# Optimization experiments

Hardware: AMD Instinct MI355X
Metric: run time of the kernel (lower is better)

Reference implementation:

```python
import jax, jax.numpy as jnp
import numpy as np

B, S, D = 4, 1024, 1024
H, DK, DH = 16, 64, 64  # num_heads, key_size, head_size
NEG = 1e12


def setup_inputs() -> dict:
    key = jax.random.key(0)
    ks = jax.random.split(key, 16)
    scale = 0.02
    inp = {
        'q': jax.random.normal(ks[0], (B, S, D), jnp.float32),
        'k': jax.random.normal(ks[1], (B, S, D), jnp.float32),
        'v': jax.random.normal(ks[2], (B, S, D), jnp.float32),
        'v_mask': jax.random.randint(ks[3], (B, S), 0, 2, jnp.int32),
        'q_mask': jax.random.randint(ks[4], (B, S), 0, 2, jnp.int32),
        # causal attention mask (float, 1 = keep)
        'a_mask': jnp.tril(jnp.ones((S, S), jnp.float32))[None, None, :, :],
        'Wq': jax.random.normal(ks[5], (D, H * DK), jnp.float32) * scale,
        'bq': jnp.zeros((H * DK,), jnp.float32),
        'Wk': jax.random.normal(ks[6], (D, H * DK), jnp.float32) * scale,
        'bk': jnp.zeros((H * DK,), jnp.float32),
        'Wv': jax.random.normal(ks[7], (D, H * DH), jnp.float32) * scale,
        'bv': jnp.zeros((H * DH,), jnp.float32),
        'Wo': jax.random.normal(ks[8], (H * DH, H * DH), jnp.float32) * scale,
        'bo': jnp.zeros((H * DH,), jnp.float32),
    }
    return inp


def reference(q, k, v, v_mask, q_mask, a_mask, Wq, bq, Wk, bk, Wv, bv, Wo, bo):
    b, sq, _ = q.shape
    sk = k.shape[1]
    qw = (jnp.einsum('bsd,de->bse', q, Wq) + bq).reshape(b, sq, H, DK)
    kw = (jnp.einsum('bsd,de->bse', k, Wk) + bk).reshape(b, sk, H, DK)
    vw = (jnp.einsum('bsd,de->bse', v, Wv) + bv).reshape(b, sk, H, DH)
    # scores [b, h, sq, sk]
    a = jnp.einsum('bjhd,bkhd->bhjk', qw, kw) / jnp.sqrt(jnp.float32(DK))
    vm = v_mask.astype(jnp.float32)  # [b, sk]
    a = a - (1.0 - vm)[:, None, None, :] * NEG  # sequence_masking mode='add'
    a = a - (1.0 - a_mask) * NEG                # attention mask
    p = jax.nn.softmax(a, axis=-1)
    o = jnp.einsum('bhjk,bkhd->bjhd', p, vw).reshape(b, sq, H * DH)
    o = jnp.einsum('bse,ef->bsf', o, Wo) + bo
    qm = q_mask.astype(jnp.float32)
    o = o * qm[:, :, None]  # sequence_masking mode='mul'
    return o
```

## Files before the change

### kernel.cpp

```cpp
#include <hip/hip_runtime.h>
#include <cstdint>
#include <cstddef>

typedef unsigned short u16;
using short8 = __attribute__((ext_vector_type(8))) short;
using f32x4  = __attribute__((ext_vector_type(4))) float;

constexpr int Sc = 1024;
constexpr float PEN = 60.0f;

__device__ __forceinline__ u16 f2bf(float f) {
  union { float f; uint32_t u; } v; v.f = f;
  return (u16)((v.u + 0x7fffu + ((v.u >> 16) & 1u)) >> 16);
}

__device__ __forceinline__ void gload_lds16(const u16* g, u16* l) {
  __builtin_amdgcn_global_load_lds(
      (const __attribute__((address_space(1))) uint32_t*)g,
      (__attribute__((address_space(3))) uint32_t*)l, 16, 0, 0);
}

__device__ __forceinline__ f32x4 mfma16(short8 a, short8 b, f32x4 c) {
  return __builtin_amdgcn_mfma_f32_16x16x32_bf16(a, b, c, 0, 0, 0);
}

__global__ __launch_bounds__(256) void prep(
    const float* __restrict__ q, const float* __restrict__ k,
    const float* __restrict__ v, u16* __restrict__ qb, u16* __restrict__ kb,
    u16* __restrict__ vb, const float* __restrict__ W0,
    const float* __restrict__ W1, const float* __restrict__ W2,
    const float* __restrict__ W3, u16* __restrict__ D0, u16* __restrict__ D1,
    u16* __restrict__ D2, u16* __restrict__ D3) {
  const int y = blockIdx.y;
  if (y < 3) {
    const float* src = y == 0 ? q : y == 1 ? k : v;
    u16* dst = y == 0 ? qb : y == 1 ? kb : vb;
    int i = blockIdx.x * 256 + threadIdx.x;
    float4 a = ((const float4*)src)[2 * i];
    float4 b = ((const float4*)src)[2 * i + 1];
    u16 t[8] = {f2bf(a.x), f2bf(a.y), f2bf(a.z), f2bf(a.w),
                f2bf(b.x), f2bf(b.y), f2bf(b.z), f2bf(b.w)};
    ((uint4*)dst)[i] = *(const uint4*)t;
  } else {
    if (blockIdx.x >= 1024) return;
    const int z = y - 3;
    const float* W = z == 0 ? W0 : z == 1 ? W1 : z == 2 ? W2 : W3;
    u16* WT = z == 0 ? D0 : z == 1 ? D1 : z == 2 ? D2 : D3;
    __shared__ float t[32][33];
    int bx = (blockIdx.x & 31) * 32, by = (blockIdx.x >> 5) * 32;
    int tx = threadIdx.x & 31, ty = threadIdx.x >> 5;
    for (int i = 0; i < 32; i += 8)
      t[ty + i][tx] = W[(size_t)(by + ty + i) * 1024 + bx + tx];
    __syncthreads();
    for (int i = 0; i < 32; i += 8)
      WT[(size_t)(bx + ty + i) * 1024 + by + tx] = f2bf(t[tx][ty + i]);
  }
}

__global__ __launch_bounds__(256, 6) void gemm_qkv(
    const u16* __restrict__ qb, const u16* __restrict__ kb,
    const u16* __restrict__ vb, const u16* __restrict__ BT,
    const float* __restrict__ bq, const float* __restrict__ bk,
    const float* __restrict__ bv, u16* __restrict__ QW, u16* __restrict__ KW,
    u16* __restrict__ VTg) {
  const int bid = blockIdx.x;
  const int xcd = bid & 7, local = bid >> 3;
  const int mp = local & 3, nbi = local >> 2;
  const int m0 = (xcd * 4 + mp) * 128, n0 = nbi * 64;
  const int seg = nbi >> 4;
  const u16* A    = seg == 0 ? qb : seg == 1 ? kb : vb;
  const float* bias = seg == 0 ? bq : seg == 1 ? bk : bv;

  __shared__ u16 As0[128 * 32], As1[128 * 32];
  __shared__ u16 Bs0[64 * 32], Bs1[64 * 32];

  const int t = threadIdx.x, w = t >> 6, lane = t & 63;
  const int q4 = lane >> 4, lm = lane & 15;
  const int wm = (w >> 1) * 64, wn = (w & 1) * 32;
  const int srow = lane >> 2, p = lane & 3;
  const int cf = q4 ^ ((lm >> 2) & 3);

  const int rbA0 = (w * 2) * 16, rbA1 = (w * 2 + 1) * 16, rbB = w * 16;
  const int rowA0 = rbA0 + srow, rowA1 = rbA1 + srow, rowB = rbB + srow;
  const int cA0 = p ^ ((rowA0 >> 2) & 3), cA1 = p ^ ((rowA1 >> 2) & 3);
  const int cB = p ^ ((rowB >> 2) & 3);
  const u16* pa0 = &A[(size_t)(m0 + rowA0) * 1024 + cA0 * 8];
  const u16* pa1 = &A[(size_t)(m0 + rowA1) * 1024 + cA1 * 8];
  const u16* pb  = &BT[(size_t)(n0 + rowB) * 1024 + cB * 8];

  f32x4 acc[4][2] = {};

  auto stage = [&](u16* as, u16* bs) {
    gload_lds16(pa0, as + rbA0 * 32);
    gload_lds16(pa1, as + rbA1 * 32);
    gload_lds16(pb, bs + rbB * 32);
    pa0 += 32; pa1 += 32; pb += 32;
  };
  auto compute = [&](const u16* as, const u16* bs) {
    short8 af[4], bf[2];
    for (int mi = 0; mi < 4; ++mi)
      af[mi] = *(const short8*)&as[(wm + mi * 16 + lm) * 32 + cf * 8];
    for (int ni = 0; ni < 2; ++ni)
      bf[ni] = *(const short8*)&bs[(wn + ni * 16 + lm) * 32 + cf * 8];
    for (int mi = 0; mi < 4; ++mi)
      for (int ni = 0; ni < 2; ++ni)
        acc[mi][ni] = mfma16(af[mi], bf[ni], acc[mi][ni]);
  };

  stage(As0, Bs0);
  for (int it = 0; it < 16; ++it) {
    __syncthreads();
    stage(As1, Bs1);
    compute(As0, Bs0);
    __syncthreads();
    if (it < 15) stage(As0, Bs0);
    compute(As1, Bs1);
  }

  if (seg < 2) {
    u16* C = seg == 0 ? QW : KW;
    for (int mi = 0; mi < 4; ++mi)
      for (int ni = 0; ni < 2; ++ni)
        for (int r = 0; r < 4; ++r) {
          int row = m0 + wm + mi * 16 + q4 * 4 + r;
          int col = (n0 + wn + ni * 16 + lm) & 1023;
          C[(size_t)row * 1024 + col] = f2bf(acc[mi][ni][r] + bias[col]);
        }
  } else {
    for (int mi = 0; mi < 4; ++mi)
      for (int ni = 0; ni < 2; ++ni) {
        int row0 = m0 + wm + mi * 16 + q4 * 4;
        int col = (n0 + wn + ni * 16 + lm) & 1023;
        float bv4 = bias[col];
        u16 o4[4];
        for (int r = 0; r < 4; ++r) o4[r] = f2bf(acc[mi][ni][r] + bv4);
        *(uint2*)&VTg[(size_t)col * 4096 + row0] = *(const uint2*)o4;
      }
  }
}

__global__ __launch_bounds__(256, 4) void gemm_out(
    const u16* __restrict__ A, const u16* __restrict__ BT,
    const float* __restrict__ bias, const int* __restrict__ qmask,
    float* __restrict__ Cf) {
  const int bid = blockIdx.x;
  const int xcd = bid & 7, local = bid >> 3;
  const int mp = local & 7, nb = local >> 3;
  const int m0 = (xcd * 8 + mp) * 64, n0 = nb * 64;

  __shared__ u16 As0[64 * 32], As1[64 * 32];
  __shared__ u16 Bs0[64 * 32], Bs1[64 * 32];
  const int t = threadIdx.x, w = t >> 6, lane = t & 63;
  const int q4 = lane >> 4, lm = lane & 15;
  const int wm = (w >> 1) * 32, wn = (w & 1) * 32;
  const int srow = lane >> 2, p = lane & 3;
  const int cf = q4 ^ ((lm >> 2) & 3);

  const int rb = w * 16;
  const int rowS = rb + srow;
  const int cS = p ^ ((rowS >> 2) & 3);
  const u16* pa = &A[(size_t)(m0 + rowS) * 1024 + cS * 8];
  const u16* pb = &BT[(size_t)(n0 + rowS) * 1024 + cS * 8];

  f32x4 acc[2][2] = {};

  auto stage = [&](u16* as, u16* bs) {
    gload_lds16(pa, as + rb * 32);
    gload_lds16(pb, bs + rb * 32);
    pa += 32; pb += 32;
  };
  auto compute = [&](const u16* as, const u16* bs) {
    short8 af[2], bf[2];
    for (int mi = 0; mi < 2; ++mi)
      af[mi] = *(const short8*)&as[(wm + mi * 16 + lm) * 32 + cf * 8];
    for (int ni = 0; ni < 2; ++ni)
      bf[ni] = *(const short8*)&bs[(wn + ni * 16 + lm) * 32 + cf * 8];
    for (int mi = 0; mi < 2; ++mi)
      for (int ni = 0; ni < 2; ++ni)
        acc[mi][ni] = mfma16(af[mi], bf[ni], acc[mi][ni]);
  };

  stage(As0, Bs0);
  for (int it = 0; it < 16; ++it) {
    __syncthreads();
    stage(As1, Bs1);
    compute(As0, Bs0);
    __syncthreads();
    if (it < 15) stage(As0, Bs0);
    compute(As1, Bs1);
  }

  for (int mi = 0; mi < 2; ++mi)
    for (int ni = 0; ni < 2; ++ni)
      for (int r = 0; r < 4; ++r) {
        int row = m0 + wm + mi * 16 + q4 * 4 + r;
        int col = n0 + wn + ni * 16 + lm;
        Cf[(size_t)row * 1024 + col] =
            (acc[mi][ni][r] + bias[col]) * (float)qmask[row];
      }
}

__global__ __launch_bounds__(256) void attn(
    const u16* __restrict__ QW, const u16* __restrict__ KW,
    const u16* __restrict__ VTg, const int* __restrict__ vmask,
    u16* __restrict__ O) {
  const int bid = blockIdx.x;
  const int xcd = bid & 7, local = bid >> 3;
  const int pair = xcd * 8 + (local & 7);
  const int b = pair >> 4, h = pair & 15;
  const int bx = local >> 3;
  const int qta = bx, qtb = 15 - bx;
  const int t = threadIdx.x, w = t >> 6, lane = t & 63;
  const int q4 = lane >> 4, lm = lane & 15;

  __shared__ u16 Ks[2][64 * 64];
  __shared__ u16 VTs[2][64 * 64];
  __shared__ u16 P[4][16 * 88];
  __shared__ float penv[1024];
  __shared__ int anyf[2];

  if (t < 2) anyf[t] = 0;
  {
    int4 vm = ((const int4*)(vmask + b * 1024))[t];
    penv[4 * t + 0] = (1.f - (float)vm.x) * PEN;
    penv[4 * t + 1] = (1.f - (float)vm.y) * PEN;
    penv[4 * t + 2] = (1.f - (float)vm.z) * PEN;
    penv[4 * t + 3] = (1.f - (float)vm.w) * PEN;
  }
  __syncthreads();
  {
    int any_a = 0, any_b = 0;
    for (int i = t; i <= qtb * 64; i += 256) {
      int un = (penv[i] == 0.f);
      if (i <= qta * 64) any_a |= un;
      any_b |= un;
    }
    if (any_a) atomicOr(&anyf[0], 1);
    if (any_b) atomicOr(&anyf[1], 1);
  }
  __syncthreads();
  const int extA = !anyf[0], extB = !anyf[1];
  const int kend = (extA || extB) ? 15 : qtb;

  short8 qf[2][2];
  for (int s = 0; s < 2; ++s) {
    int qt = s ? qtb : qta;
    const u16* qp = &QW[(size_t)(b * Sc + qt * 64 + w * 16 + lm) * 1024 + h * 64];
    qf[s][0] = *(const short8*)&qp[q4 * 8];
    qf[s][1] = *(const short8*)&qp[32 + q4 * 8];
    for (int fi = 0; fi < 2; ++fi)
      for (int i = 0; i < 8; ++i) {
        u16 x = (u16)qf[s][fi][i];
        int e = (x >> 7) & 0xff;
        qf[s][fi][i] = (short)(e > 3 ? (u16)(x - 0x180) : (u16)(x & 0x8000));
      }
  }

  float l_run[2][4] = {};
  f32x4 oacc[2][4] = {};

  const int r0 = lane >> 3, pos = lane & 7, ch = pos ^ r0;
  auto stage = [&](int kt, int buf) {
    for (int j = 0; j < 2; ++j) {
      int issue = w * 2 + j;
      int row = issue * 8 + r0;
      gload_lds16(&KW[(size_t)(b * Sc + kt * 64 + row) * 1024 + h * 64 + ch * 8],
                  &Ks[buf][issue * 512]);
      gload_lds16(&VTg[(size_t)(h * 64 + row) * 4096 + b * Sc + kt * 64 + ch * 8],
                  &VTs[buf][issue * 512]);
    }
  };

  auto strip_tile = [&](int s, int kt, int mode, int buf) {
    const int qt = s ? qtb : qta;
    const int qrow0 = qt * 64 + w * 16 + q4 * 4;
    f32x4 sacc[4] = {};
    for (int ni = 0; ni < 4; ++ni) {
      int row = ni * 16 + lm;
      short8 kf0 = *(const short8*)&Ks[buf][row * 64 + ((q4 ^ (lm & 7)) * 8)];
      short8 kf1 = *(const short8*)&Ks[buf][row * 64 + (((4 + q4) ^ (lm & 7)) * 8)];
      sacc[ni] = mfma16(qf[s][0], kf0, sacc[ni]);
      sacc[ni] = mfma16(qf[s][1], kf1, sacc[ni]);
    }
    u16* Pw = &P[w][0];
    for (int ni = 0; ni < 4; ++ni) {
      int key = kt * 64 + ni * 16 + lm;
      float pen = penv[key];
      if (mode == 2) pen += PEN;
      for (int r = 0; r < 4; ++r) {
        float x = sacc[ni][r] - pen;
        if (mode == 1 && key > qrow0 + r) x -= PEN;
        float pv = __expf(x);
        l_run[s][r] += pv;
        Pw[(q4 * 4 + r) * 88 + ni * 16 + lm] = f2bf(pv);
      }
    }
    short8 pf0 = *(const short8*)&Pw[lm * 88 + q4 * 8];
    short8 pf1 = *(const short8*)&Pw[lm * 88 + 32 + q4 * 8];
    for (int ni = 0; ni < 4; ++ni) {
      int row = ni * 16 + lm;
      short8 vf0 = *(const short8*)&VTs[buf][row * 64 + ((q4 ^ (lm & 7)) * 8)];
      short8 vf1 = *(const short8*)&VTs[buf][row * 64 + (((4 + q4) ^ (lm & 7)) * 8)];
      oacc[s][ni] = mfma16(pf0, vf0, oacc[s][ni]);
      oacc[s][ni] = mfma16(pf1, vf1, oacc[s][ni]);
    }
  };

  stage(0, 0);
  int cur = 0;
  for (int kt = 0; kt <= kend; ++kt) {
    __syncthreads();
    if (kt < kend) stage(kt + 1, cur ^ 1);
    if (kt <= qta) strip_tile(0, kt, kt == qta ? 1 : 0, cur);
    else if (extA) strip_tile(0, kt, 2, cur);
    if (kt <= qtb) strip_tile(1, kt, kt == qtb ? 1 : 0, cur);
    else if (extB) strip_tile(1, kt, 2, cur);
    cur ^= 1;
  }

  for (int s = 0; s < 2; ++s) {
    int qt = s ? qtb : qta;
    for (int r = 0; r < 4; ++r) {
      float l = l_run[s][r];
      for (int off = 1; off < 16; off <<= 1) l += __shfl_xor(l, off, 64);
      l_run[s][r] = 1.0f / l;
    }
    for (int ni = 0; ni < 4; ++ni)
      for (int r = 0; r < 4; ++r) {
        int row = b * Sc + qt * 64 + w * 16 + q4 * 4 + r;
        O[(size_t)row * 1024 + h * 64 + ni * 16 + lm] =
            f2bf(oacc[s][ni][r] * l_run[s][r]);
      }
  }
}

extern "C" void kernel_launch(void* const* d_in, const int* in_sizes, int n_in,
                              void* d_out, int out_size, void* d_ws, size_t ws_size,
                              hipStream_t stream) {
  (void)in_sizes; (void)n_in; (void)out_size; (void)ws_size;
  const float* q  = (const float*)d_in[0];
  const float* k  = (const float*)d_in[1];
  const float* v  = (const float*)d_in[2];
  const int* vmask = (const int*)d_in[3];
  const int* qmask = (const int*)d_in[4];
  const float* Wq = (const float*)d_in[6];
  const float* bq = (const float*)d_in[7];
  const float* Wk = (const float*)d_in[8];
  const float* bk = (const float*)d_in[9];
  const float* Wv = (const float*)d_in[10];
  const float* bv = (const float*)d_in[11];
  const float* Wo = (const float*)d_in[12];
  const float* bo = (const float*)d_in[13];

  char* ws = (char*)d_ws;
  u16* WT3 = (u16*)ws;
  u16* WoT = (u16*)(ws + 6291456);
  u16* QW  = (u16*)(ws + 8388608);
  u16* KW  = (u16*)(ws + 16777216);
  u16* VTg = (u16*)(ws + 25165824);
  u16* Oat = (u16*)(ws + 33554432);
  u16* qb = (u16*)d_out;
  u16* kb = (u16*)d_out + 4194304;
  u16* vb = Oat;

  dim3 tb(256);
  prep<<<dim3(2048, 7), tb, 0, stream>>>(q, k, v, qb, kb, vb, Wq, Wk, Wv, Wo,
                                         WT3, WT3 + 1048576, WT3 + 2097152,
                                         WoT);
  gemm_qkv<<<dim3(1536), tb, 0, stream>>>(qb, kb, vb, WT3, bq, bk, bv, QW, KW,
                                          VTg);
  attn<<<dim3(512), tb, 0, stream>>>(QW, KW, VTg, vmask, Oat);
  gemm_out<<<dim3(1024), tb, 0, stream>>>(Oat, WoT, bo, qmask, (float*)d_out);
}
```

Measured before the change: 221.8 us.

## Split attention into one q-tile per block, reading K/V from global directly

The attention kernel now launches one block per (batch, head, q-tile) instead of pairing complementary q-tiles in one block. Blocks are ordered so the longest causal tiles go first. K and V^T fragments are loaded straight from global memory into registers, replacing the double-buffered LDS staging and per-tile barriers. A 4-blocks-per-CU launch bound is added. This aims for more parallelism and occupancy without LDS traffic or syncs, at the cost of uncoalesced, redundant global reads (each wave re-reads K/V) and losing the load-balancing tile pairing and the xcd-aware mapping.

```diff
diff --git a/kernel.cpp b/kernel.cpp
--- a/kernel.cpp
+++ b/kernel.cpp
@@ -200,26 +200,23 @@
       }
 }
 
-__global__ __launch_bounds__(256) void attn(
+__global__ __launch_bounds__(256, 4) void attn(
     const u16* __restrict__ QW, const u16* __restrict__ KW,
     const u16* __restrict__ VTg, const int* __restrict__ vmask,
     u16* __restrict__ O) {
   const int bid = blockIdx.x;
-  const int xcd = bid & 7, local = bid >> 3;
-  const int pair = xcd * 8 + (local & 7);
-  const int b = pair >> 4, h = pair & 15;
-  const int bx = local >> 3;
-  const int qta = bx, qtb = 15 - bx;
+  const int qtidx = bid >> 6;
+  const int qt = qtidx == 0 ? 0 : 16 - qtidx;
+  const int pi = bid & 63;
+  const int b = pi >> 4, h = pi & 15;
   const int t = threadIdx.x, w = t >> 6, lane = t & 63;
   const int q4 = lane >> 4, lm = lane & 15;
 
-  __shared__ u16 Ks[2][64 * 64];
-  __shared__ u16 VTs[2][64 * 64];
   __shared__ u16 P[4][16 * 88];
   __shared__ float penv[1024];
-  __shared__ int anyf[2];
-
-  if (t < 2) anyf[t] = 0;
+  __shared__ int anyf;
+
+  if (t == 0) anyf = 0;
   {
     int4 vm = ((const int4*)(vmask + b * 1024))[t];
     penv[4 * t + 0] = (1.f - (float)vm.x) * PEN;
@@ -229,60 +226,54 @@
   }
   __syncthreads();
   {
-    int any_a = 0, any_b = 0;
-    for (int i = t; i <= qtb * 64; i += 256) {
-      int un = (penv[i] == 0.f);
-      if (i <= qta * 64) any_a |= un;
-      any_b |= un;
-    }
-    if (any_a) atomicOr(&anyf[0], 1);
-    if (any_b) atomicOr(&anyf[1], 1);
+    int any = 0;
+    for (int i = t; i <= qt * 64; i += 256) any |= (penv[i] == 0.f);
+    if (any) atomicOr(&anyf, 1);
   }
   __syncthreads();
-  const int extA = !anyf[0], extB = !anyf[1];
-  const int kend = (extA || extB) ? 15 : qtb;
-
-  short8 qf[2][2];
-  for (int s = 0; s < 2; ++s) {
-    int qt = s ? qtb : qta;
+  const int ext = !anyf;
+  const int kend = ext ? 15 : qt;
+
+  short8 qf[2];
+  {
     const u16* qp = &QW[(size_t)(b * Sc + qt * 64 + w * 16 + lm) * 1024 + h * 64];
-    qf[s][0] = *(const short8*)&qp[q4 * 8];
-    qf[s][1] = *(const short8*)&qp[32 + q4 * 8];
+    qf[0] = *(const short8*)&qp[q4 * 8];
+    qf[1] = *(const short8*)&qp[32 + q4 * 8];
     for (int fi = 0; fi < 2; ++fi)
       for (int i = 0; i < 8; ++i) {
-        u16 x = (u16)qf[s][fi][i];
+        u16 x = (u16)qf[fi][i];
         int e = (x >> 7) & 0xff;
-        qf[s][fi][i] = (short)(e > 3 ? (u16)(x - 0x180) : (u16)(x & 0x8000));
+        qf[fi][i] = (short)(e > 3 ? (u16)(x - 0x180) : (u16)(x & 0x8000));
       }
   }
 
-  float l_run[2][4] = {};
-  f32x4 oacc[2][4] = {};
-
-  const int r0 = lane >> 3, pos = lane & 7, ch = pos ^ r0;
-  auto stage = [&](int kt, int buf) {
-    for (int j = 0; j < 2; ++j) {
-      int issue = w * 2 + j;
-      int row = issue * 8 + r0;
-      gload_lds16(&KW[(size_t)(b * Sc + kt * 64 + row) * 1024 + h * 64 + ch * 8],
-                  &Ks[buf][issue * 512]);
-      gload_lds16(&VTg[(size_t)(h * 64 + row) * 4096 + b * Sc + kt * 64 + ch * 8],
-                  &VTs[buf][issue * 512]);
-    }
-  };
-
-  auto strip_tile = [&](int s, int kt, int mode, int buf) {
-    const int qt = s ? qtb : qta;
-    const int qrow0 = qt * 64 + w * 16 + q4 * 4;
+  float l_run[4] = {};
+  f32x4 oacc[4] = {};
+  const int qrow0 = qt * 64 + w * 16 + q4 * 4;
+
+  const u16* Kbase = &KW[(size_t)(b * Sc) * 1024 + h * 64];
+  const u16* Vbase = &VTg[(size_t)(h * 64) * 4096 + b * Sc];
+  u16* Pw = &P[w][0];
+
+  for (int kt = 0; kt <= kend; ++kt) {
+    const int mode = kt > qt ? 2 : (kt == qt ? 1 : 0);
+
     f32x4 sacc[4] = {};
     for (int ni = 0; ni < 4; ++ni) {
-      int row = ni * 16 + lm;
-      short8 kf0 = *(const short8*)&Ks[buf][row * 64 + ((q4 ^ (lm & 7)) * 8)];
-      short8 kf1 = *(const short8*)&Ks[buf][row * 64 + (((4 + q4) ^ (lm & 7)) * 8)];
-      sacc[ni] = mfma16(qf[s][0], kf0, sacc[ni]);
-      sacc[ni] = mfma16(qf[s][1], kf1, sacc[ni]);
-    }
-    u16* Pw = &P[w][0];
+      const u16* kp = Kbase + (size_t)(kt * 64 + ni * 16 + lm) * 1024;
+      short8 kf0 = *(const short8*)&kp[q4 * 8];
+      short8 kf1 = *(const short8*)&kp[32 + q4 * 8];
+      sacc[ni] = mfma16(qf[0], kf0, sacc[ni]);
+      sacc[ni] = mfma16(qf[1], kf1, sacc[ni]);
+    }
+
+    short8 vf0[4], vf1[4];
+    for (int ni = 0; ni < 4; ++ni) {
+      const u16* vp = Vbase + (size_t)(ni * 16 + lm) * 4096 + kt * 64;
+      vf0[ni] = *(const short8*)&vp[q4 * 8];
+      vf1[ni] = *(const short8*)&vp[32 + q4 * 8];
+    }
+
     for (int ni = 0; ni < 4; ++ni) {
       int key = kt * 64 + ni * 16 + lm;
       float pen = penv[key];
@@ -291,47 +282,29 @@
         float x = sacc[ni][r] - pen;
         if (mode == 1 && key > qrow0 + r) x -= PEN;
         float pv = __expf(x);
-        l_run[s][r] += pv;
+        l_run[r] += pv;
         Pw[(q4 * 4 + r) * 88 + ni * 16 + lm] = f2bf(pv);
       }
     }
     short8 pf0 = *(const short8*)&Pw[lm * 88 + q4 * 8];
     short8 pf1 = *(const short8*)&Pw[lm * 88 + 32 + q4 * 8];
     for (int ni = 0; ni < 4; ++ni) {
-      int row = ni * 16 + lm;
-      short8 vf0 = *(const short8*)&VTs[buf][row * 64 + ((q4 ^ (lm & 7)) * 8)];
-      short8 vf1 = *(const short8*)&VTs[buf][row * 64 + (((4 + q4) ^ (lm & 7)) * 8)];
-      oacc[s][ni] = mfma16(pf0, vf0, oacc[s][ni]);
-      oacc[s][ni] = mfma16(pf1, vf1, oacc[s][ni]);
-    }
-  };
-
-  stage(0, 0);
-  int cur = 0;
-  for (int kt = 0; kt <= kend; ++kt) {
-    __syncthreads();
-    if (kt < kend) stage(kt + 1, cur ^ 1);
-    if (kt <= qta) strip_tile(0, kt, kt == qta ? 1 : 0, cur);
-    else if (extA) strip_tile(0, kt, 2, cur);
-    if (kt <= qtb) strip_tile(1, kt, kt == qtb ? 1 : 0, cur);
-    else if (extB) strip_tile(1, kt, 2, cur);
-    cur ^= 1;
-  }
-
-  for (int s = 0; s < 2; ++s) {
-    int qt = s ? qtb : qta;
+      oacc[ni] = mfma16(pf0, vf0[ni], oacc[ni]);
+      oacc[ni] = mfma16(pf1, vf1[ni], oacc[ni]);
+    }
+  }
+
+  for (int r = 0; r < 4; ++r) {
+    float l = l_run[r];
+    for (int off = 1; off < 16; off <<= 1) l += __shfl_xor(l, off, 64);
+    l_run[r] = 1.0f / l;
+  }
+  for (int ni = 0; ni < 4; ++ni)
     for (int r = 0; r < 4; ++r) {
-      float l = l_run[s][r];
-      for (int off = 1; off < 16; off <<= 1) l += __shfl_xor(l, off, 64);
-      l_run[s][r] = 1.0f / l;
-    }
-    for (int ni = 0; ni < 4; ++ni)
-      for (int r = 0; r < 4; ++r) {
-        int row = b * Sc + qt * 64 + w * 16 + q4 * 4 + r;
-        O[(size_t)row * 1024 + h * 64 + ni * 16 + lm] =
-            f2bf(oacc[s][ni][r] * l_run[s][r]);
-      }
-  }
+      int row = b * Sc + qt * 64 + w * 16 + q4 * 4 + r;
+      O[(size_t)row * 1024 + h * 64 + ni * 16 + lm] =
+          f2bf(oacc[ni][r] * l_run[r]);
+    }
 }
 
 extern "C" void kernel_launch(void* const* d_in, const int* in_sizes, int n_in,
@@ -369,6 +342,6 @@
                                          WoT);
   gemm_qkv<<<dim3(1536), tb, 0, stream>>>(qb, kb, vb, WT3, bq, bk, bv, QW, KW,
                                           VTg);
-  attn<<<dim3(512), tb, 0, stream>>>(QW, KW, VTg, vmask, Oat);
+  attn<<<dim3(1024), tb, 0, stream>>>(QW, KW, VTg, vmask, Oat);
   gemm_out<<<dim3(1024), tb, 0, stream>>>(Oat, WoT, bo, qmask, (float*)d_out);
 }
```

Result: slower. 262.0 us (+18.1%).
